# Kernel tuning notes

Measured on AMD Instinct MI355X. Metric: run time of the kernel, lower is better.

Reference implementation:

```python
import jax, jax.numpy as jnp
import numpy as np

B, L, H, E, M = 8, 1024, 1024, 2048, 2048  # batch, seq, hidden_dim, expanded_dim, max_seq_length


def setup_inputs() -> dict:
    key = jax.random.key(0)
    ks = jax.random.split(key, 10)
    n = lambda k, shape, s=0.02: jax.random.normal(k, shape, jnp.float32) * s
    return {
        'x': jax.random.normal(ks[0], (B, L, H), jnp.float32),
        'ln1_w': jnp.ones((H,), jnp.float32), 'ln1_b': jnp.zeros((H,), jnp.float32),
        'ln2_w': jnp.ones((E,), jnp.float32), 'ln2_b': jnp.zeros((E,), jnp.float32),
        'w_qkv': n(ks[1], (3 * E, H)), 'b_qkv': jnp.zeros((3 * E,), jnp.float32),
        'w_out': n(ks[2], (H, E)), 'b_out': jnp.zeros((H,), jnp.float32),
        'rel_pos': n(ks[3], (2 * M - 1, H)),
        'w_beta': n(ks[4], (E, 2 * H)), 'b_beta': jnp.zeros((E,), jnp.float32),
        'w1': n(ks[5], (4 * H, H)), 'b1': jnp.zeros((4 * H,), jnp.float32),
        'w2': n(ks[6], (H, 4 * H)), 'b2': jnp.zeros((H,), jnp.float32),
        'conv_w': n(ks[7], (E, 1, 3), 0.3),  # depthwise conv1d weight [C,1,K]
        'attn_scale': jnp.ones((1,), jnp.float32),
    }


def _ln(x, w, b):
    m = jnp.mean(x, -1, keepdims=True)
    v = jnp.mean((x - m) ** 2, -1, keepdims=True)
    return (x - m) / jnp.sqrt(v + 1e-5) * w + b


def _normalize(x):
    # F.normalize(x, dim=-1): x / max(||x||_2, 1e-12)
    return x / jnp.maximum(jnp.linalg.norm(x, axis=-1, keepdims=True), 1e-12)


def _dwconv(z, w):
    # z: [B,L,E]; depthwise conv1d k=3, pad=1, no bias (groups=E)
    y = jax.lax.conv_general_dilated(
        z.transpose(0, 2, 1), w, window_strides=(1,), padding=((1, 1),),
        feature_group_count=w.shape[0], dimension_numbers=('NCH', 'OIH', 'NCH'))
    return y.transpose(0, 2, 1)


def reference(x, ln1_w, ln1_b, ln2_w, ln2_b, w_qkv, b_qkv, w_out, b_out,
              rel_pos, w_beta, b_beta, w1, b1, w2, b2, conv_w, attn_scale):
    Lx = x.shape[1]
    h = _ln(x, ln1_w, ln1_b)
    qkv = h @ w_qkv.T + b_qkv
    q, k, v = jnp.split(qkv, 3, axis=-1)  # each [B,L,E]
    q = jax.nn.silu(q)
    k = jax.nn.silu(k)
    v = jax.nn.gelu(v, approximate=False)
    # interdependent normalize-mix (k uses the updated q)
    q = _normalize(q) + 0.1 * k
    k = _normalize(k) + 0.1 * q
    q = _dwconv(q, conv_w)
    k = _dwconv(k, conv_w)
    v = _dwconv(v, conv_w)
    # position-conditioned beta gate
    pos_embed = rel_pos[:Lx]  # [L,H]
    pos_info = jnp.einsum('blh,mh->blm', h, pos_embed).mean(-1, keepdims=True)  # [B,L,1]
    comb = jnp.concatenate([h, jnp.broadcast_to(pos_info, h.shape)], axis=-1)  # [B,L,2H]
    beta = jax.nn.sigmoid(comb @ w_beta.T + b_beta) * 0.9 + 0.1  # [B,L,E]
    # delta-rule: state starts at zeros so v_old = state @ k^T = 0 exactly
    v_new = beta * v  # beta*v + (1-beta)*0
    state = jnp.einsum('ble,blf->bef', v_new, k)  # v_new^T @ k : [B,E,E]
    out = jnp.einsum('ble,bfe->blf', q, state) * attn_scale  # q @ state^T
    out = _ln(out, ln2_w, ln2_b) @ w_out.T + b_out
    x = x + out
    h2 = _ln(x, ln1_w, ln1_b)  # norm1 is reused pre-MLP
    mlp = jax.nn.gelu(h2 @ w1.T + b1, approximate=False) @ w2.T + b2
    return x + mlp
```

## Files before the change

### kernel.cpp

```cpp
#include <hip/hip_runtime.h>
#include <hip/hip_bf16.h>
#include <math.h>

using bf16 = __hip_bfloat16;
typedef __attribute__((ext_vector_type(8))) short bf16x8;
typedef __attribute__((ext_vector_type(4))) float f32x4;

#define DEVI __device__ __forceinline__

DEVI float b2f(bf16 v) { return __bfloat162float(v); }
DEVI bf16 f2b(float v) { return __float2bfloat16(v); }
DEVI float geluf(float x) { return 0.5f * x * (1.0f + erff(x * 0.70710678118654752f)); }
DEVI float siluf(float x) { return x / (1.0f + expf(-x)); }

DEVI void load_lds16(const bf16* g, bf16* l) {
  __builtin_amdgcn_global_load_lds(
      (const __attribute__((address_space(1))) void*)g,
      (__attribute__((address_space(3))) void*)l, 16, 0, 0);
}

__global__ __launch_bounds__(256) void cast_kernel(const float* __restrict__ in,
                                                   bf16* __restrict__ out, int n4) {
  int i = blockIdx.x * 256 + threadIdx.x;
  if (i >= n4) return;
  float4 v = reinterpret_cast<const float4*>(in)[i];
  bf16 o[4] = { f2b(v.x), f2b(v.y), f2b(v.z), f2b(v.w) };
  reinterpret_cast<uint2*>(out)[i] = *reinterpret_cast<uint2*>(o);
}

__global__ __launch_bounds__(256) void pmean_kernel(const float* __restrict__ rel,
                                                    float* __restrict__ pm) {
  int h = blockIdx.x * 256 + threadIdx.x;
  float s = 0.f;
  for (int m = 0; m < 1024; ++m) s += rel[m * 1024 + h];
  pm[h] = s * (1.0f / 1024.0f);
}

__global__ __launch_bounds__(64) void wb2sum_kernel(const float* __restrict__ wb,
                                                    float* __restrict__ out) {
  int e = blockIdx.x;
  float s = 0.f;
  for (int j = threadIdx.x; j < 1024; j += 64) s += wb[(long)e * 2048 + 1024 + j];
#pragma unroll
  for (int off = 32; off > 0; off >>= 1) s += __shfl_down(s, off);
  if (threadIdx.x == 0) out[e] = s;
}

__global__ __launch_bounds__(256) void convw_pack_kernel(const float* __restrict__ cw,
                                                         bf16* __restrict__ wpl) {
  int e = blockIdx.x * 256 + threadIdx.x;
  wpl[e]        = f2b(cw[e * 3]);
  wpl[2048 + e] = f2b(cw[e * 3 + 1]);
  wpl[4096 + e] = f2b(cw[e * 3 + 2]);
}

template<bool POS>
__global__ __launch_bounds__(256) void ln1024_kernel(
    const float* __restrict__ x, const float* __restrict__ w, const float* __restrict__ b,
    bf16* __restrict__ out, const float* __restrict__ pmean, float* __restrict__ pos) {
  __shared__ float red[12];
  long row = blockIdx.x;
  int t = threadIdx.x, lane = t & 63, wid = t >> 6;
  float4 xv = reinterpret_cast<const float4*>(x + row * 1024)[t];
  float s = xv.x + xv.y + xv.z + xv.w;
  float ss = xv.x * xv.x + xv.y * xv.y + xv.z * xv.z + xv.w * xv.w;
#pragma unroll
  for (int off = 32; off > 0; off >>= 1) { s += __shfl_down(s, off); ss += __shfl_down(ss, off); }
  if (lane == 0) { red[wid] = s; red[4 + wid] = ss; }
  __syncthreads();
  s = red[0] + red[1] + red[2] + red[3];
  ss = red[4] + red[5] + red[6] + red[7];
  float mean = s * (1.0f / 1024.0f);
  float rstd = rsqrtf(ss * (1.0f / 1024.0f) - mean * mean + 1e-5f);
  float4 wv = reinterpret_cast<const float4*>(w)[t];
  float4 bv = reinterpret_cast<const float4*>(b)[t];
  float h0 = (xv.x - mean) * rstd * wv.x + bv.x;
  float h1 = (xv.y - mean) * rstd * wv.y + bv.y;
  float h2 = (xv.z - mean) * rstd * wv.z + bv.z;
  float h3 = (xv.w - mean) * rstd * wv.w + bv.w;
  bf16 o[4] = { f2b(h0), f2b(h1), f2b(h2), f2b(h3) };
  reinterpret_cast<uint2*>(out + row * 1024)[t] = *reinterpret_cast<uint2*>(o);
  if (POS) {
    float4 pv = reinterpret_cast<const float4*>(pmean)[t];
    float d = h0 * pv.x + h1 * pv.y + h2 * pv.z + h3 * pv.w;
#pragma unroll
    for (int off = 32; off > 0; off >>= 1) d += __shfl_down(d, off);
    if (lane == 0) red[8 + wid] = d;
    __syncthreads();
    if (t == 0) pos[row] = red[8] + red[9] + red[10] + red[11];
  }
}

__global__ __launch_bounds__(256) void ln2048_bf16_kernel(
    const bf16* __restrict__ in, const float* __restrict__ w, const float* __restrict__ b,
    bf16* __restrict__ out) {
  __shared__ float red[8];
  long row = blockIdx.x;
  int t = threadIdx.x, lane = t & 63, wid = t >> 6;
  bf16 tv[8];
  *reinterpret_cast<int4*>(tv) = reinterpret_cast<const int4*>(in + row * 2048)[t];
  float v[8], s = 0.f, ss = 0.f;
#pragma unroll
  for (int j = 0; j < 8; ++j) { v[j] = b2f(tv[j]); s += v[j]; ss += v[j] * v[j]; }
#pragma unroll
  for (int off = 32; off > 0; off >>= 1) { s += __shfl_down(s, off); ss += __shfl_down(ss, off); }
  if (lane == 0) { red[wid] = s; red[4 + wid] = ss; }
  __syncthreads();
  s = red[0] + red[1] + red[2] + red[3];
  ss = red[4] + red[5] + red[6] + red[7];
  float mean = s * (1.0f / 2048.0f);
  float rstd = rsqrtf(ss * (1.0f / 2048.0f) - mean * mean + 1e-5f);
  int base = t * 8;
  bf16 o[8];
#pragma unroll
  for (int j = 0; j < 8; ++j) o[j] = f2b((v[j] - mean) * rstd * w[base + j] + b[base + j]);
  reinterpret_cast<int4*>(out + row * 2048)[t] = *reinterpret_cast<int4*>(o);
}

__global__ __launch_bounds__(256) void act_norm_kernel(
    bf16* __restrict__ qp, bf16* __restrict__ kp, bf16* __restrict__ vp) {
  __shared__ float red[8];
  long row = blockIdx.x;
  int t = threadIdx.x, lane = t & 63, wid = t >> 6;
  long ob = row * 2048 + t * 8;
  bf16 tq[8], tk[8], tv[8];
  *reinterpret_cast<int4*>(tq) = *reinterpret_cast<const int4*>(qp + ob);
  *reinterpret_cast<int4*>(tk) = *reinterpret_cast<const int4*>(kp + ob);
  *reinterpret_cast<int4*>(tv) = *reinterpret_cast<const int4*>(vp + ob);
  float qs[8], ks[8];
  float sq = 0.f, sk = 0.f;
#pragma unroll
  for (int j = 0; j < 8; ++j) {
    float q = b2f(tq[j]); qs[j] = siluf(q); sq += qs[j] * qs[j];
    float k = b2f(tk[j]); ks[j] = siluf(k); sk += ks[j] * ks[j];
  }
#pragma unroll
  for (int off = 32; off > 0; off >>= 1) { sq += __shfl_down(sq, off); sk += __shfl_down(sk, off); }
  if (lane == 0) { red[wid] = sq; red[4 + wid] = sk; }
  __syncthreads();
  sq = red[0] + red[1] + red[2] + red[3];
  sk = red[4] + red[5] + red[6] + red[7];
  float rq = 1.0f / fmaxf(sqrtf(sq), 1e-12f);
  float rk = 1.0f / fmaxf(sqrtf(sk), 1e-12f);
  bf16 oq[8], ok[8], ov[8];
#pragma unroll
  for (int j = 0; j < 8; ++j) {
    float qn = qs[j] * rq + 0.1f * ks[j];
    float kn = ks[j] * rk + 0.1f * qn;
    oq[j] = f2b(qn); ok[j] = f2b(kn);
    ov[j] = f2b(geluf(b2f(tv[j])));
  }
  *reinterpret_cast<int4*>(qp + ob) = *reinterpret_cast<int4*>(oq);
  *reinterpret_cast<int4*>(kp + ob) = *reinterpret_cast<int4*>(ok);
  *reinterpret_cast<int4*>(vp + ob) = *reinterpret_cast<int4*>(ov);
}

__global__ __launch_bounds__(256) void dwconv_kernel(
    const bf16* __restrict__ in, bf16* __restrict__ out, const bf16* __restrict__ wpl) {
  const int t = threadIdx.x;
  const int e0 = t * 8;
  const long bl = blockIdx.x;
  const int l = (int)(bl & 1023);
  const bf16* mid = in + (bl * 2048 + e0);
  bf16 tm[8], tp[8], tn[8], w0[8], w1[8], w2[8];
  *reinterpret_cast<int4*>(tm) = *reinterpret_cast<const int4*>(mid);
  if (l > 0)    *reinterpret_cast<int4*>(tp) = *reinterpret_cast<const int4*>(mid - 2048);
  if (l < 1023) *reinterpret_cast<int4*>(tn) = *reinterpret_cast<const int4*>(mid + 2048);
  *reinterpret_cast<int4*>(w0) = *reinterpret_cast<const int4*>(&wpl[e0]);
  *reinterpret_cast<int4*>(w1) = *reinterpret_cast<const int4*>(&wpl[2048 + e0]);
  *reinterpret_cast<int4*>(w2) = *reinterpret_cast<const int4*>(&wpl[4096 + e0]);
  bf16 o[8];
#pragma unroll
  for (int j = 0; j < 8; ++j) {
    float a = b2f(w1[j]) * b2f(tm[j]);
    if (l > 0) a += b2f(w0[j]) * b2f(tp[j]);
    if (l < 1023) a += b2f(w2[j]) * b2f(tn[j]);
    o[j] = f2b(a);
  }
  *reinterpret_cast<int4*>(out + (bl * 2048 + e0)) = *reinterpret_cast<int4*>(o);
}

__global__ __launch_bounds__(256) void transpose2f_kernel(
    const bf16* __restrict__ in1, bf16* __restrict__ out1,
    const bf16* __restrict__ in2, bf16* __restrict__ out2,
    const bf16* __restrict__ wpl) {
  const int zz = blockIdx.z;
  const bool isk = (zz < 8);
  const bf16* in = isk ? in1 : in2;
  bf16* out = isk ? out1 : out2;
  const long base = (long)(zz & 7) * 2097152;
  const int r0 = blockIdx.y * 64 + ((threadIdx.x & 63) >> 3) * 8;
  const int c0 = blockIdx.x * 256 + (threadIdx.x >> 6) * 64 + (threadIdx.x & 7) * 8;
  bf16 vv[8][8];
  if (isk) {
    bf16 raw[10][8];
#pragma unroll
    for (int j = 0; j < 10; ++j) {
      int r = r0 + j - 1;
      if (r >= 0 && r < 1024)
        *reinterpret_cast<int4*>(raw[j]) =
            *reinterpret_cast<const int4*>(&in[base + (long)r * 2048 + c0]);
      else {
#pragma unroll
        for (int i = 0; i < 8; ++i) raw[j][i] = f2b(0.f);
      }
    }
    bf16 w0[8], w1[8], w2[8];
    *reinterpret_cast<int4*>(w0) = *reinterpret_cast<const int4*>(&wpl[c0]);
    *reinterpret_cast<int4*>(w1) = *reinterpret_cast<const int4*>(&wpl[2048 + c0]);
    *reinterpret_cast<int4*>(w2) = *reinterpret_cast<const int4*>(&wpl[4096 + c0]);
#pragma unroll
    for (int j = 0; j < 8; ++j)
#pragma unroll
      for (int i = 0; i < 8; ++i)
        vv[j][i] = f2b(b2f(w0[i]) * b2f(raw[j][i]) + b2f(w1[i]) * b2f(raw[j + 1][i]) +
                       b2f(w2[i]) * b2f(raw[j + 2][i]));
  } else {
#pragma unroll
    for (int j = 0; j < 8; ++j)
      *reinterpret_cast<int4*>(vv[j]) =
          *reinterpret_cast<const int4*>(&in[base + (long)(r0 + j) * 2048 + c0]);
  }
#pragma unroll
  for (int i = 0; i < 8; ++i) {
    bf16 w[8];
#pragma unroll
    for (int j = 0; j < 8; ++j) w[j] = vv[j][i];
    *reinterpret_cast<int4*>(&out[base + (long)(c0 + i) * 1024 + r0]) =
        *reinterpret_cast<int4*>(w);
  }
}

enum { EPI_QKV = 0, EPI_BETA = 1, EPI_BF16 = 2, EPI_SCALE = 3, EPI_RES_F32 = 4, EPI_GELU = 5 };

#define MF(d, a, b) d = __builtin_amdgcn_mfma_f32_16x16x32_bf16(a, b, d, 0, 0, 0)
#define RD_A(S, MR, KK) \
  (*reinterpret_cast<const bf16x8*>(&smem[(S)*16384 + wm*8192 + ((MR)*16 + r16)*64 + ((((KK)*32) + kq8) ^ swz)]))
#define RD_B(S, NR, KK) \
  (*reinterpret_cast<const bf16x8*>(&smem[32768 + (S)*16384 + (wn>>1)*8192 + ((wn&1)*64 + (NR)*16 + r16)*64 + ((((KK)*32) + kq8) ^ swz)]))
#define STAGE_A1(S, H, Q, KT) \
  load_lds16(Abase + (long)((H)*128 + (Q)*64) * lda + (long)(KT)*64, \
             &smem[(S)*16384 + (H)*8192 + (Q)*4096 + wid*512])
#define STAGE_B1(S, H, Q, KT) \
  load_lds16(Bbase + (long)((H)*128 + (Q)*64) * ldb + (long)(KT)*64, \
             &smem[32768 + (S)*16384 + (H)*8192 + (Q)*4096 + wid*512])
#define STAGE_AH(S, H, KT) { STAGE_A1(S, H, 0, KT); STAGE_A1(S, H, 1, KT); }
#define STAGE_BH(S, H, KT) { STAGE_B1(S, H, 0, KT); STAGE_B1(S, H, 1, KT); }
#define BAR_A __builtin_amdgcn_s_barrier()
#define LGKM0 { asm volatile("s_waitcnt lgkmcnt(0)" ::: "memory"); __builtin_amdgcn_sched_barrier(0); }
#define VWAIT(LST) { if (LST) { asm volatile("s_waitcnt vmcnt(0)" ::: "memory"); } \
                     else     { asm volatile("s_waitcnt vmcnt(6)" ::: "memory"); } \
                     __builtin_amdgcn_sched_barrier(0); }

#define KTILE(S, ST1, ST2, ST3, ST4, W4) { \
  bf16x8 aL[4][2], aH[4][2], bL[2][2], bH[2][2]; \
  _Pragma("unroll") for (int m_ = 0; m_ < 4; ++m_) { aL[m_][0] = RD_A(S, m_, 0); aL[m_][1] = RD_A(S, m_, 1); } \
  _Pragma("unroll") for (int n_ = 0; n_ < 2; ++n_) { bL[n_][0] = RD_B(S, n_, 0); bL[n_][1] = RD_B(S, n_, 1); } \
  ST1; BAR_A; LGKM0; \
  __builtin_amdgcn_s_setprio(1); \
  _Pragma("unroll") for (int m_ = 0; m_ < 4; ++m_) _Pragma("unroll") for (int n_ = 0; n_ < 2; ++n_) { \
    MF(acc[m_][n_], aL[m_][0], bL[n_][0]); MF(acc[m_][n_], aL[m_][1], bL[n_][1]); } \
  __builtin_amdgcn_s_setprio(0); __builtin_amdgcn_s_barrier(); \
  _Pragma("unroll") for (int n_ = 0; n_ < 2; ++n_) { bH[n_][0] = RD_B(S, n_ + 2, 0); bH[n_][1] = RD_B(S, n_ + 2, 1); } \
  ST2; BAR_A; LGKM0; \
  __builtin_amdgcn_s_setprio(1); \
  _Pragma("unroll") for (int m_ = 0; m_ < 4; ++m_) _Pragma("unroll") for (int n_ = 0; n_ < 2; ++n_) { \
    MF(acc[m_][n_ + 2], aL[m_][0], bH[n_][0]); MF(acc[m_][n_ + 2], aL[m_][1], bH[n_][1]); } \
  __builtin_amdgcn_s_setprio(0); __builtin_amdgcn_s_barrier(); \
  _Pragma("unroll") for (int m_ = 0; m_ < 4; ++m_) { aH[m_][0] = RD_A(S, m_ + 4, 0); aH[m_][1] = RD_A(S, m_ + 4, 1); } \
  ST3; BAR_A; LGKM0; \
  __builtin_amdgcn_s_setprio(1); \
  _Pragma("unroll") for (int m_ = 0; m_ < 4; ++m_) _Pragma("unroll") for (int n_ = 0; n_ < 2; ++n_) { \
    MF(acc[m_ + 4][n_], aH[m_][0], bL[n_][0]); MF(acc[m_ + 4][n_], aH[m_][1], bL[n_][1]); } \
  __builtin_amdgcn_s_setprio(0); __builtin_amdgcn_s_barrier(); \
  ST4; W4; BAR_A; LGKM0; \
  __builtin_amdgcn_s_setprio(1); \
  _Pragma("unroll") for (int m_ = 0; m_ < 4; ++m_) _Pragma("unroll") for (int n_ = 0; n_ < 2; ++n_) { \
    MF(acc[m_ + 4][n_ + 2], aH[m_][0], bH[n_][0]); MF(acc[m_ + 4][n_ + 2], aH[m_][1], bH[n_][1]); } \
  __builtin_amdgcn_s_setprio(0); __builtin_amdgcn_s_barrier(); \
}

template<int EPI>
__global__ __launch_bounds__(512) void gemm256_kernel(
    const bf16* __restrict__ A, int lda, long sA,
    const bf16* __restrict__ B, int ldb, long sB,
    void* __restrict__ Cv, int ldc, long sC, int K,
    const float* __restrict__ bias, const float* __restrict__ aux_row,
    const float* __restrict__ aux_col, const bf16* __restrict__ vconv,
    const float* __restrict__ resid, const float* __restrict__ scale_ptr,
    bf16* __restrict__ p2, bf16* __restrict__ p3) {
  __shared__ bf16 smem[65536];
  const int bz = blockIdx.z;
  A += (long)bz * sA;
  B += (long)bz * sB;
  const int m0 = blockIdx.y * 256, n0 = blockIdx.x * 256;
  const int t = threadIdx.x, lane = t & 63, wid = t >> 6;
  const int wm = wid >> 2, wn = wid & 3;
  const int r16 = lane & 15, kq8 = (lane >> 4) * 8;
  const int swz = (r16 & 7) << 3;
  const int lrow = lane >> 3;
  const int cswz = ((lane & 7) ^ lrow) * 8;
  const bf16* Abase = A + (long)(m0 + wid * 8 + lrow) * lda + cswz;
  const bf16* Bbase = B + (long)(n0 + wid * 8 + lrow) * ldb + cswz;
  f32x4 acc[8][4] = {};
  const int NT = K >> 6, NIT = NT >> 1;
  STAGE_AH(0, 0, 0); STAGE_AH(0, 1, 0); STAGE_BH(0, 0, 0); STAGE_BH(0, 1, 0);
  STAGE_BH(1, 0, 1); STAGE_BH(1, 1, 1); STAGE_AH(1, 0, 1);
  asm volatile("s_waitcnt vmcnt(6)" ::: "memory");
  __builtin_amdgcn_sched_barrier(0);
  __builtin_amdgcn_s_barrier();
  for (int i = 0; i < NIT; ++i) {
    const int tb = 2 * i;
    const bool lst = (i == NIT - 1);
    KTILE(0,
      { STAGE_AH(1, 1, tb + 1); },
      { },
      { if (!lst) { STAGE_BH(0, 0, tb + 2); STAGE_BH(0, 1, tb + 2); } },
      { if (!lst) { STAGE_AH(0, 0, tb + 2); } },
      VWAIT(lst));
    KTILE(1,
      { if (!lst) { STAGE_AH(0, 1, tb + 2); } },
      { },
      { if (!lst) { STAGE_BH(1, 0, tb + 3); STAGE_BH(1, 1, tb + 3); } },
      { if (!lst) { STAGE_AH(1, 0, tb + 3); } },
      VWAIT(lst));
  }
  float scl = 1.0f;
  if (EPI == EPI_SCALE) scl = scale_ptr[0];
  const int rb = (lane >> 4) * 4;
#pragma unroll
  for (int mr = 0; mr < 8; ++mr) {
#pragma unroll
    for (int nr = 0; nr < 4; ++nr) {
#pragma unroll
      for (int r = 0; r < 4; ++r) {
        const long gm = m0 + wm * 128 + mr * 16 + rb + r;
        const int gn = n0 + wn * 64 + nr * 16 + r16;
        const long idx = (long)bz * sC + gm * (long)ldc + gn;
        float v = acc[mr][nr][r];
        if (EPI == EPI_QKV) {
          const int seg = gn >> 11, cc = gn & 2047;
          bf16* dst = (seg == 0) ? (bf16*)Cv : (seg == 1) ? p2 : p3;
          dst[gm * 2048 + cc] = f2b(v + bias[gn]);
        } else if (EPI == EPI_BETA) {
          float tt = v + bias[gn] + aux_row[gm] * aux_col[gn];
          float be = 0.9f / (1.0f + expf(-tt)) + 0.1f;
          ((bf16*)Cv)[idx] = f2b(be * b2f(vconv[idx]));
        } else if (EPI == EPI_BF16) {
          ((bf16*)Cv)[idx] = f2b(v);
        } else if (EPI == EPI_SCALE) {
          ((bf16*)Cv)[idx] = f2b(v * scl);
        } else if (EPI == EPI_RES_F32) {
          ((float*)Cv)[idx] = v + bias[gn] + resid[idx];
        } else {
          ((bf16*)Cv)[idx] = f2b(geluf(v + bias[gn]));
        }
      }
    }
  }
}

#define A_RD(S, MR, KK) \
  (*reinterpret_cast<const bf16x8*>(&amem[(S)*8192 + (wm*64 + (MR)*16 + r16)*64 + ((((KK)*32) + kq8) ^ swz)]))
#define B_RD(S, NR, KK) \
  (*reinterpret_cast<const bf16x8*>(&amem[16384 + (S)*16384 + (wn*64 + (NR)*16 + r16)*64 + ((((KK)*32) + kq8) ^ swz)]))
#define A_ST(S, Q, KT) \
  load_lds16(Abase + (long)((Q)*64) * lda + (long)(KT)*64, &amem[(S)*8192 + (Q)*4096 + wid*512])
#define B_ST(S, Q, KT) \
  load_lds16(Bbase + (long)((Q)*64) * ldb + (long)(KT)*64, &amem[16384 + (S)*16384 + (Q)*4096 + wid*512])
#define STAGE_T(S, KT) { A_ST(S, 0, KT); A_ST(S, 1, KT); B_ST(S, 0, KT); B_ST(S, 1, KT); B_ST(S, 2, KT); B_ST(S, 3, KT); }

__global__ __launch_bounds__(512) void gemmA128_kernel(
    const bf16* __restrict__ A, int lda,
    const bf16* __restrict__ B, int ldb,
    float* __restrict__ C, int ldc, int K,
    const float* __restrict__ bias, const float* __restrict__ resid) {
  __shared__ bf16 amem[49152];
  const int m0 = blockIdx.y * 128, n0 = blockIdx.x * 256;
  const int t = threadIdx.x, lane = t & 63, wid = t >> 6;
  const int wm = wid >> 2, wn = wid & 3;
  const int r16 = lane & 15, kq8 = (lane >> 4) * 8;
  const int swz = (r16 & 7) << 3;
  const int lrow = lane >> 3;
  const int cswz = ((lane & 7) ^ lrow) * 8;
  const bf16* Abase = A + (long)(m0 + wid * 8 + lrow) * lda + cswz;
  const bf16* Bbase = B + (long)(n0 + wid * 8 + lrow) * ldb + cswz;
  f32x4 acc[4][4] = {};
  const int NT = K >> 6;
  STAGE_T(0, 0); STAGE_T(1, 1);
  asm volatile("s_waitcnt vmcnt(6)" ::: "memory");
  __builtin_amdgcn_sched_barrier(0);
  __builtin_amdgcn_s_barrier();
  for (int tt = 0; tt < NT; ++tt) {
    const int S = tt & 1;
    const bool pre = (tt + 2 < NT);
    bf16x8 a[4][2], bL[2][2], bH[2][2];
#pragma unroll
    for (int m_ = 0; m_ < 4; ++m_) { a[m_][0] = A_RD(S, m_, 0); a[m_][1] = A_RD(S, m_, 1); }
#pragma unroll
    for (int n_ = 0; n_ < 2; ++n_) { bL[n_][0] = B_RD(S, n_, 0); bL[n_][1] = B_RD(S, n_, 1); }
#pragma unroll
    for (int n_ = 0; n_ < 2; ++n_) { bH[n_][0] = B_RD(S, n_ + 2, 0); bH[n_][1] = B_RD(S, n_ + 2, 1); }
    LGKM0;
    __builtin_amdgcn_s_setprio(1);
#pragma unroll
    for (int m_ = 0; m_ < 4; ++m_)
#pragma unroll
      for (int n_ = 0; n_ < 2; ++n_) {
        MF(acc[m_][n_], a[m_][0], bL[n_][0]); MF(acc[m_][n_], a[m_][1], bL[n_][1]);
      }
    __builtin_amdgcn_s_setprio(0);
    __builtin_amdgcn_s_barrier();
    __builtin_amdgcn_sched_barrier(0);
    if (pre) STAGE_T(S, tt + 2);
    __builtin_amdgcn_s_setprio(1);
#pragma unroll
    for (int m_ = 0; m_ < 4; ++m_)
#pragma unroll
      for (int n_ = 0; n_ < 2; ++n_) {
        MF(acc[m_][n_ + 2], a[m_][0], bH[n_][0]); MF(acc[m_][n_ + 2], a[m_][1], bH[n_][1]);
      }
    __builtin_amdgcn_s_setprio(0);
    if (pre) { asm volatile("s_waitcnt vmcnt(6)" ::: "memory"); }
    else     { asm volatile("s_waitcnt vmcnt(0)" ::: "memory"); }
    __builtin_amdgcn_sched_barrier(0);
    __builtin_amdgcn_s_barrier();
    __builtin_amdgcn_sched_barrier(0);
  }
  const int rb = (lane >> 4) * 4;
#pragma unroll
  for (int mr = 0; mr < 4; ++mr) {
#pragma unroll
    for (int nr = 0; nr < 4; ++nr) {
#pragma unroll
      for (int r = 0; r < 4; ++r) {
        const long gm = m0 + wm * 64 + mr * 16 + rb + r;
        const int gn = n0 + wn * 64 + nr * 16 + r16;
        const long idx = gm * (long)ldc + gn;
        C[idx] = acc[mr][nr][r] + bias[gn] + resid[idx];
      }
    }
  }
}

extern "C" void kernel_launch(void* const* d_in, const int* in_sizes, int n_in,
                              void* d_out, int out_size, void* d_ws, size_t ws_size,
                              hipStream_t stream) {
  (void)in_sizes; (void)n_in; (void)out_size;
  const float* x       = (const float*)d_in[0];
  const float* ln1_w   = (const float*)d_in[1];
  const float* ln1_b   = (const float*)d_in[2];
  const float* ln2_w   = (const float*)d_in[3];
  const float* ln2_b   = (const float*)d_in[4];
  const float* w_qkv   = (const float*)d_in[5];
  const float* b_qkv   = (const float*)d_in[6];
  const float* w_out   = (const float*)d_in[7];
  const float* b_out   = (const float*)d_in[8];
  const float* rel_pos = (const float*)d_in[9];
  const float* w_beta  = (const float*)d_in[10];
  const float* b_beta  = (const float*)d_in[11];
  const float* w1      = (const float*)d_in[12];
  const float* b1      = (const float*)d_in[13];
  const float* w2      = (const float*)d_in[14];
  const float* b2      = (const float*)d_in[15];
  const float* conv_w  = (const float*)d_in[16];
  const float* attn_sc = (const float*)d_in[17];
  float* out = (float*)d_out;

  if (ws_size < 180400128UL) return;
  char* ws = (char*)d_ws;
  bf16*  wbuf    = (bf16*)(ws + 0);
  bf16*  wpl     = (bf16*)(ws + 10485760UL);
  float* pmean   = (float*)(ws + 12582912UL);
  float* wb2s    = (float*)(ws + 12587008UL);
  float* posinfo = (float*)(ws + 12595200UL);
  bf16* R0 = (bf16*)(ws + 12627968UL);
  bf16* R1 = (bf16*)(ws + 46182400UL);
  bf16* R2 = (bf16*)(ws + 79736832UL);
  bf16* R3 = (bf16*)(ws + 113291264UL);
  bf16* R4 = (bf16*)(ws + 146845696UL);
  float* x2 = (float*)R1;

  pmean_kernel<<<4, 256, 0, stream>>>(rel_pos, pmean);
  wb2sum_kernel<<<2048, 64, 0, stream>>>(w_beta, wb2s);

  ln1024_kernel<true><<<8192, 256, 0, stream>>>(x, ln1_w, ln1_b, R0, pmean, posinfo);

  cast_kernel<<<6144, 256, 0, stream>>>(w_qkv, wbuf, 1572864);
  gemm256_kernel<EPI_QKV><<<dim3(24, 32, 1), 512, 0, stream>>>(
      R0, 1024, 0, wbuf, 1024, 0, R1, 2048, 0, 1024,
      b_qkv, nullptr, nullptr, nullptr, nullptr, nullptr, R2, R3);

  act_norm_kernel<<<8192, 256, 0, stream>>>(R1, R2, R3);

  convw_pack_kernel<<<8, 256, 0, stream>>>(conv_w, wpl);
  dwconv_kernel<<<8192, 256, 0, stream>>>(R1, R4, wpl);
  dwconv_kernel<<<8192, 256, 0, stream>>>(R3, R1, wpl);

  cast_kernel<<<4096, 256, 0, stream>>>(w_beta, wbuf, 1048576);
  gemm256_kernel<EPI_BETA><<<dim3(8, 32, 1), 512, 0, stream>>>(
      R0, 1024, 0, wbuf, 2048, 0, R1, 2048, 0, 1024,
      b_beta, posinfo, wb2s, R1, nullptr, nullptr, nullptr, nullptr);

  transpose2f_kernel<<<dim3(8, 16, 16), 256, 0, stream>>>(R2, R3, R1, R0, wpl);

  gemm256_kernel<EPI_BF16><<<dim3(8, 8, 8), 512, 0, stream>>>(
      R0, 1024, 2097152, R3, 1024, 2097152, R1, 2048, 4194304, 1024,
      nullptr, nullptr, nullptr, nullptr, nullptr, nullptr, nullptr, nullptr);

  gemm256_kernel<EPI_SCALE><<<dim3(8, 4, 8), 512, 0, stream>>>(
      R4, 2048, 2097152, R1, 2048, 4194304, R3, 2048, 2097152, 2048,
      nullptr, nullptr, nullptr, nullptr, nullptr, attn_sc, nullptr, nullptr);

  ln2048_bf16_kernel<<<8192, 256, 0, stream>>>(R3, ln2_w, ln2_b, R0);

  cast_kernel<<<2048, 256, 0, stream>>>(w_out, wbuf, 524288);
  gemmA128_kernel<<<dim3(4, 64, 1), 512, 0, stream>>>(
      R0, 2048, wbuf, 2048, x2, 1024, 2048, b_out, x);

  ln1024_kernel<false><<<8192, 256, 0, stream>>>(x2, ln1_w, ln1_b, R2, nullptr, nullptr);

  cast_kernel<<<4096, 256, 0, stream>>>(w1, wbuf, 1048576);
  gemm256_kernel<EPI_GELU><<<dim3(16, 32, 1), 512, 0, stream>>>(
      R2, 1024, 0, wbuf, 1024, 0, R3, 4096, 0, 1024,
      b1, nullptr, nullptr, nullptr, nullptr, nullptr, nullptr, nullptr);

  cast_kernel<<<4096, 256, 0, stream>>>(w2, wbuf, 1048576);
  gemmA128_kernel<<<dim3(4, 64, 1), 512, 0, stream>>>(
      R3, 4096, wbuf, 4096, out, 1024, 4096, b2, x2);
}
```

Before: 751.6 us.

## Store residual stream in bf16, merge prep and dwconv launches, reuse output as scratch

Merges the two small preparation kernels into a single launch and the two dwconv launches into one 2D grid. The v-conv result is written into the output buffer as scratch. The intermediate residual x2 is now stored as bf16 rather than fp32, which halves its write and its two later reads, and adds a bf16-input LayerNorm kernel for it. The trade-off is lower precision on the residual path, since x2 feeds the final output through the second residual add.

```diff
diff --git a/kernel.cpp b/kernel.cpp
--- a/kernel.cpp
+++ b/kernel.cpp
@@ -28,22 +28,25 @@
   reinterpret_cast<uint2*>(out)[i] = *reinterpret_cast<uint2*>(o);
 }
 
-__global__ __launch_bounds__(256) void pmean_kernel(const float* __restrict__ rel,
-                                                    float* __restrict__ pm) {
-  int h = blockIdx.x * 256 + threadIdx.x;
-  float s = 0.f;
-  for (int m = 0; m < 1024; ++m) s += rel[m * 1024 + h];
-  pm[h] = s * (1.0f / 1024.0f);
-}
-
-__global__ __launch_bounds__(64) void wb2sum_kernel(const float* __restrict__ wb,
-                                                    float* __restrict__ out) {
-  int e = blockIdx.x;
-  float s = 0.f;
-  for (int j = threadIdx.x; j < 1024; j += 64) s += wb[(long)e * 2048 + 1024 + j];
-#pragma unroll
-  for (int off = 32; off > 0; off >>= 1) s += __shfl_down(s, off);
-  if (threadIdx.x == 0) out[e] = s;
+__global__ __launch_bounds__(256) void prep_kernel(const float* __restrict__ rel,
+                                                   float* __restrict__ pm,
+                                                   const float* __restrict__ wb,
+                                                   float* __restrict__ wb2s) {
+  const int b = blockIdx.x;
+  if (b < 4) {
+    int h = b * 256 + threadIdx.x;
+    float s = 0.f;
+    for (int m = 0; m < 1024; ++m) s += rel[m * 1024 + h];
+    pm[h] = s * (1.0f / 1024.0f);
+  } else {
+    int e = (b - 4) * 4 + (threadIdx.x >> 6);
+    int lane = threadIdx.x & 63;
+    float s = 0.f;
+    for (int j = lane; j < 1024; j += 64) s += wb[(long)e * 2048 + 1024 + j];
+#pragma unroll
+    for (int off = 32; off > 0; off >>= 1) s += __shfl_down(s, off);
+    if (lane == 0) wb2s[e] = s;
+  }
 }
 
 __global__ __launch_bounds__(256) void convw_pack_kernel(const float* __restrict__ cw,
@@ -91,6 +94,35 @@
   }
 }
 
+__global__ __launch_bounds__(256) void ln1024b_kernel(
+    const bf16* __restrict__ x, const float* __restrict__ w, const float* __restrict__ b,
+    bf16* __restrict__ out) {
+  __shared__ float red[8];
+  long row = blockIdx.x;
+  int t = threadIdx.x, lane = t & 63, wid = t >> 6;
+  bf16 tv[4];
+  *reinterpret_cast<uint2*>(tv) = reinterpret_cast<const uint2*>(x + row * 1024)[t];
+  float v[4], s = 0.f, ss = 0.f;
+#pragma unroll
+  for (int j = 0; j < 4; ++j) { v[j] = b2f(tv[j]); s += v[j]; ss += v[j] * v[j]; }
+#pragma unroll
+  for (int off = 32; off > 0; off >>= 1) { s += __shfl_down(s, off); ss += __shfl_down(ss, off); }
+  if (lane == 0) { red[wid] = s; red[4 + wid] = ss; }
+  __syncthreads();
+  s = red[0] + red[1] + red[2] + red[3];
+  ss = red[4] + red[5] + red[6] + red[7];
+  float mean = s * (1.0f / 1024.0f);
+  float rstd = rsqrtf(ss * (1.0f / 1024.0f) - mean * mean + 1e-5f);
+  float4 wv = reinterpret_cast<const float4*>(w)[t];
+  float4 bv = reinterpret_cast<const float4*>(b)[t];
+  bf16 o[4];
+  o[0] = f2b((v[0] - mean) * rstd * wv.x + bv.x);
+  o[1] = f2b((v[1] - mean) * rstd * wv.y + bv.y);
+  o[2] = f2b((v[2] - mean) * rstd * wv.z + bv.z);
+  o[3] = f2b((v[3] - mean) * rstd * wv.w + bv.w);
+  reinterpret_cast<uint2*>(out + row * 1024)[t] = *reinterpret_cast<uint2*>(o);
+}
+
 __global__ __launch_bounds__(256) void ln2048_bf16_kernel(
     const bf16* __restrict__ in, const float* __restrict__ w, const float* __restrict__ b,
     bf16* __restrict__ out) {
@@ -155,8 +187,12 @@
   *reinterpret_cast<int4*>(vp + ob) = *reinterpret_cast<int4*>(ov);
 }
 
-__global__ __launch_bounds__(256) void dwconv_kernel(
-    const bf16* __restrict__ in, bf16* __restrict__ out, const bf16* __restrict__ wpl) {
+__global__ __launch_bounds__(256) void dwconv2_kernel(
+    const bf16* __restrict__ q_in, bf16* __restrict__ q_out,
+    const bf16* __restrict__ v_in, bf16* __restrict__ v_out,
+    const bf16* __restrict__ wpl) {
+  const bf16* in = blockIdx.y ? v_in : q_in;
+  bf16* out = blockIdx.y ? v_out : q_out;
   const int t = threadIdx.x;
   const int e0 = t * 8;
   const long bl = blockIdx.x;
@@ -370,11 +406,12 @@
   load_lds16(Bbase + (long)((Q)*64) * ldb + (long)(KT)*64, &amem[16384 + (S)*16384 + (Q)*4096 + wid*512])
 #define STAGE_T(S, KT) { A_ST(S, 0, KT); A_ST(S, 1, KT); B_ST(S, 0, KT); B_ST(S, 1, KT); B_ST(S, 2, KT); B_ST(S, 3, KT); }
 
+template<int RB, int WB>
 __global__ __launch_bounds__(512) void gemmA128_kernel(
     const bf16* __restrict__ A, int lda,
     const bf16* __restrict__ B, int ldb,
-    float* __restrict__ C, int ldc, int K,
-    const float* __restrict__ bias, const float* __restrict__ resid) {
+    void* __restrict__ Cv, int ldc, int K,
+    const float* __restrict__ bias, const void* __restrict__ residv) {
   __shared__ bf16 amem[49152];
   const int m0 = blockIdx.y * 128, n0 = blockIdx.x * 256;
   const int t = threadIdx.x, lane = t & 63, wid = t >> 6;
@@ -437,7 +474,10 @@
         const long gm = m0 + wm * 64 + mr * 16 + rb + r;
         const int gn = n0 + wn * 64 + nr * 16 + r16;
         const long idx = gm * (long)ldc + gn;
-        C[idx] = acc[mr][nr][r] + bias[gn] + resid[idx];
+        float rv = RB ? b2f(((const bf16*)residv)[idx]) : ((const float*)residv)[idx];
+        float o = acc[mr][nr][r] + bias[gn] + rv;
+        if (WB) ((bf16*)Cv)[idx] = f2b(o);
+        else    ((float*)Cv)[idx] = o;
       }
     }
   }
@@ -470,7 +510,7 @@
   if (ws_size < 180400128UL) return;
   char* ws = (char*)d_ws;
   bf16*  wbuf    = (bf16*)(ws + 0);
-  bf16*  wpl     = (bf16*)(ws + 10485760UL);
+  bf16*  wpl     = (bf16*)(ws + 11534336UL);
   float* pmean   = (float*)(ws + 12582912UL);
   float* wb2s    = (float*)(ws + 12587008UL);
   float* posinfo = (float*)(ws + 12595200UL);
@@ -479,10 +519,10 @@
   bf16* R2 = (bf16*)(ws + 79736832UL);
   bf16* R3 = (bf16*)(ws + 113291264UL);
   bf16* R4 = (bf16*)(ws + 146845696UL);
-  float* x2 = (float*)R1;
-
-  pmean_kernel<<<4, 256, 0, stream>>>(rel_pos, pmean);
-  wb2sum_kernel<<<2048, 64, 0, stream>>>(w_beta, wb2s);
+  bf16* vscr = (bf16*)d_out;
+  bf16* x2b = R1;
+
+  prep_kernel<<<516, 256, 0, stream>>>(rel_pos, pmean, w_beta, wb2s);
 
   ln1024_kernel<true><<<8192, 256, 0, stream>>>(x, ln1_w, ln1_b, R0, pmean, posinfo);
 
@@ -494,13 +534,12 @@
   act_norm_kernel<<<8192, 256, 0, stream>>>(R1, R2, R3);
 
   convw_pack_kernel<<<8, 256, 0, stream>>>(conv_w, wpl);
-  dwconv_kernel<<<8192, 256, 0, stream>>>(R1, R4, wpl);
-  dwconv_kernel<<<8192, 256, 0, stream>>>(R3, R1, wpl);
+  dwconv2_kernel<<<dim3(8192, 2), 256, 0, stream>>>(R1, R4, R3, vscr, wpl);
 
   cast_kernel<<<4096, 256, 0, stream>>>(w_beta, wbuf, 1048576);
   gemm256_kernel<EPI_BETA><<<dim3(8, 32, 1), 512, 0, stream>>>(
       R0, 1024, 0, wbuf, 2048, 0, R1, 2048, 0, 1024,
-      b_beta, posinfo, wb2s, R1, nullptr, nullptr, nullptr, nullptr);
+      b_beta, posinfo, wb2s, vscr, nullptr, nullptr, nullptr, nullptr);
 
   transpose2f_kernel<<<dim3(8, 16, 16), 256, 0, stream>>>(R2, R3, R1, R0, wpl);
 
@@ -515,10 +554,10 @@
   ln2048_bf16_kernel<<<8192, 256, 0, stream>>>(R3, ln2_w, ln2_b, R0);
 
   cast_kernel<<<2048, 256, 0, stream>>>(w_out, wbuf, 524288);
-  gemmA128_kernel<<<dim3(4, 64, 1), 512, 0, stream>>>(
-      R0, 2048, wbuf, 2048, x2, 1024, 2048, b_out, x);
-
-  ln1024_kernel<false><<<8192, 256, 0, stream>>>(x2, ln1_w, ln1_b, R2, nullptr, nullptr);
+  gemmA128_kernel<0, 1><<<dim3(4, 64, 1), 512, 0, stream>>>(
+      R0, 2048, wbuf, 2048, x2b, 1024, 2048, b_out, x);
+
+  ln1024b_kernel<<<8192, 256, 0, stream>>>(x2b, ln1_w, ln1_b, R2);
 
   cast_kernel<<<4096, 256, 0, stream>>>(w1, wbuf, 1048576);
   gemm256_kernel<EPI_GELU><<<dim3(16, 32, 1), 512, 0, stream>>>(
@@ -526,6 +565,6 @@
       b1, nullptr, nullptr, nullptr, nullptr, nullptr, nullptr, nullptr);
 
   cast_kernel<<<4096, 256, 0, stream>>>(w2, wbuf, 1048576);
-  gemmA128_kernel<<<dim3(4, 64, 1), 512, 0, stream>>>(
-      R3, 4096, wbuf, 4096, out, 1024, 4096, b2, x2);
-}
+  gemmA128_kernel<1, 0><<<dim3(4, 64, 1), 512, 0, stream>>>(
+      R3, 4096, wbuf, 4096, out, 1024, 4096, b2, x2b);
+}
```

After: 732.9 us. 2.5% less time.
